# Kernel tuning notes

Measured on AMD Instinct MI355X. Metric: run time of the kernel, lower is better.

The kernel has to match this reference:

```python
import jax, jax.numpy as jnp
import numpy as np

B, S, F, EMB, HID = 64, 2048, 40, 128, 256


def setup_inputs() -> dict:
    key = jax.random.key(0)
    ks = jax.random.split(key, 12)
    sc_in = 1.0 / np.sqrt(F)
    sc_h = 1.0 / np.sqrt(HID)
    n = lambda k, shape, sc: (jax.random.normal(k, shape, jnp.float32) * sc)
    return {
        "in_states": jax.random.normal(ks[0], (B, S, F), jnp.float32),
        "W_in": n(ks[1], (EMB, F), sc_in),
        "b_in": jnp.zeros((EMB,), jnp.float32),  # bias init to 0 in original
        "W_ih0": n(ks[2], (4 * HID, EMB), sc_h),
        "W_hh0": n(ks[3], (4 * HID, HID), sc_h),
        "b_ih0": n(ks[4], (4 * HID,), sc_h),
        "b_hh0": n(ks[5], (4 * HID,), sc_h),
        "W_ih1": n(ks[6], (4 * HID, HID), sc_h),
        "W_hh1": n(ks[7], (4 * HID, HID), sc_h),
        "b_ih1": n(ks[8], (4 * HID,), sc_h),
        "b_hh1": n(ks[9], (4 * HID,), sc_h),
        "W_out": n(ks[10], (1, HID), sc_h),
        "b_out": jnp.zeros((1,), jnp.float32),  # bias init to 0 in original
    }


def _lstm_layer(x, W_ih, W_hh, b_ih, b_hh):
    # x: [B, S, D_in]; returns hs: [B, S, H], final (h, c)
    Bb = x.shape[0]
    H = W_hh.shape[1]
    # Precompute input contribution for all timesteps (one big GEMM).
    gx = jnp.einsum('bsd,gd->bsg', x, W_ih) + b_ih + b_hh  # [B, S, 4H]

    def step(carry, gxt):
        h, c = carry
        g = gxt + h @ W_hh.T  # [B, 4H]
        i, f, gg, o = jnp.split(g, 4, axis=-1)  # PyTorch gate order i,f,g,o
        i = jax.nn.sigmoid(i)
        f = jax.nn.sigmoid(f)
        gg = jnp.tanh(gg)
        o = jax.nn.sigmoid(o)
        c = f * c + i * gg
        h = o * jnp.tanh(c)
        return (h, c), h

    init = (jnp.zeros((Bb, H), x.dtype), jnp.zeros((Bb, H), x.dtype))
    (h, c), hs = jax.lax.scan(step, init, jnp.swapaxes(gx, 0, 1))
    return jnp.swapaxes(hs, 0, 1), (h, c)


def reference(in_states, W_in, b_in, W_ih0, W_hh0, b_ih0, b_hh0,
              W_ih1, W_hh1, b_ih1, b_hh1, W_out, b_out):
    # Input projection applied to every timestep (equivalent to per-step Linear).
    x = jnp.einsum('bsf,ef->bse', in_states, W_in) + b_in  # [B, S, EMB]
    y, _ = _lstm_layer(x, W_ih0, W_hh0, b_ih0, b_hh0)
    y, _ = _lstm_layer(y, W_ih1, W_hh1, b_ih1, b_hh1)
    out = jnp.einsum('bsh,oh->bso', y, W_out) + b_out  # [B, S, 1]
    return out[..., 0]  # [B, S], matches torch.t(outputs)
```

## Files before the change

### kernel.cpp

```cpp
#include <hip/hip_runtime.h>


#define Sz    2048
#define PIPE  4
#define NG    4
#define NJ    8

typedef __attribute__((ext_vector_type(8))) short short8;
typedef __attribute__((ext_vector_type(4))) float f32x4;

#define PUB0_U64 0
#define PUB1_U64 65536
#define CFLG_U32 262144
#define WS_U32   262176

#define HA_HI 0
#define HA_LO 8448
#define HB_HI 16896
#define HB_LO 25344
#define IN_HI 33792
#define IN_LO 36096
#define GBUF  38400
#define SMEM_BYTES 46848
#define WCOMB_OFF 16896

__device__ __forceinline__ unsigned short bf16_rne(float f) {
  unsigned u = __float_as_uint(f);
  u += 0x7FFFu + ((u >> 16) & 1u);
  return (unsigned short)(u >> 16);
}
__device__ __forceinline__ float sigm(float x) { return 1.f / (1.f + __expf(-x)); }
__device__ __forceinline__ float tanh_f(float x) { return 1.f - 2.f / (__expf(2.f * x) + 1.f); }

__device__ __forceinline__ bool load_stage(const unsigned long long* __restrict__ src,
                                           unsigned tagExp, char* hi, char* lo, int tid) {
  unsigned long long v[16];
#pragma unroll
  for (int kt = 0; kt < 8; ++kt) {
    v[kt * 2]     = __hip_atomic_load(src + kt * 512 + tid,       __ATOMIC_RELAXED, __HIP_MEMORY_SCOPE_AGENT);
    v[kt * 2 + 1] = __hip_atomic_load(src + kt * 512 + 256 + tid, __ATOMIC_RELAXED, __HIP_MEMORY_SCOPE_AGENT);
  }
  bool ok = true;
#pragma unroll
  for (int kt = 0; kt < 8; ++kt) {
#pragma unroll
    for (int hh = 0; hh < 2; ++hh) {
      unsigned long long x = v[kt * 2 + hh];
      ok &= ((unsigned)(x >> 32) == tagExp);
      unsigned pk = (unsigned)x;
      int e = tid + hh * 256;
      int m = e >> 5, col = kt * 32 + (e & 31);
      *(short*)(hi + m * 528 + col * 2) = (short)(pk >> 16);
      *(short*)(lo + m * 528 + col * 2) = (short)(pk & 0xffffu);
    }
  }
  return ok;
}

__global__ void zero_kernel(unsigned* __restrict__ ws, float* __restrict__ out) {
  int i = blockIdx.x * 256 + threadIdx.x;
  if (i < WS_U32) ws[i] = 0u;
  if (i < 64 * Sz) out[i] = 0.f;
}

__global__ __launch_bounds__(256, 1) void lstm_persist(
    const float* __restrict__ xin, const float* __restrict__ W_in,
    const float* __restrict__ b_in, const float* __restrict__ W_ih0,
    const float* __restrict__ W_hh0, const float* __restrict__ b_ih0,
    const float* __restrict__ b_hh0, const float* __restrict__ W_ih1,
    const float* __restrict__ W_hh1, const float* __restrict__ b_ih1,
    const float* __restrict__ b_hh1, const float* __restrict__ W_out,
    const float* __restrict__ b_out, float* __restrict__ out,
    unsigned* __restrict__ ws) {
  const int bx = blockIdx.x;
  const int g = bx & 7;
  if (g >= NG) return;
  const int idx = bx >> 3;
  const int layer = idx >> 3;
  const int p = idx & 7;
  const int tid = (int)threadIdx.x;
  const int w = tid >> 6;
  const int lane = tid & 63;
  const int q = lane >> 4;
  const int n16 = lane & 15;

  __shared__ __align__(16) char smem[SMEM_BYTES];

  const int row0 = w * 256 + p * 32 + n16;
  const int row1 = row0 + 16;

  short8 wf_rec[8][2];
  short8 wf_in2[8][2];
  short8 wf_cmb[2][2];
  float bias0 = 0.f, bias1 = 0.f;

  {
    const float* Wrec = layer ? W_hh1 : W_hh0;
#pragma unroll
    for (int kt = 0; kt < 8; ++kt) {
#pragma unroll
      for (int u = 0; u < 2; ++u) {
        const int row = u ? row1 : row0;
        const float* src = Wrec + (size_t)row * 256 + kt * 32 + q * 8;
        union { short8 v; unsigned short s[8]; } fr;
#pragma unroll
        for (int j = 0; j < 8; ++j) fr.s[j] = bf16_rne(src[j]);
        wf_rec[kt][u] = fr.v;
      }
    }
  }
  if (layer == 1) {
#pragma unroll
    for (int kt = 0; kt < 8; ++kt) {
#pragma unroll
      for (int u = 0; u < 2; ++u) {
        const int row = u ? row1 : row0;
        const float* src = W_ih1 + (size_t)row * 256 + kt * 32 + q * 8;
        union { short8 v; unsigned short s[8]; } fr;
#pragma unroll
        for (int j = 0; j < 8; ++j) fr.s[j] = bf16_rne(src[j]);
        wf_in2[kt][u] = fr.v;
      }
    }
    bias0 = b_ih1[row0] + b_hh1[row0];
    bias1 = b_ih1[row1] + b_hh1[row1];
  } else {
    float* wcomb = (float*)(smem + WCOMB_OFF);
    for (int i = tid; i < 128 * 40; i += 256) {
      int rl = i / 40, f = i - rl * 40;
      int gate = rl >> 5, rr = rl & 31;
      int arow = gate * 256 + p * 32 + rr;
      const float* wi = W_ih0 + (size_t)arow * 128;
      float s = 0.f;
      for (int e = 0; e < 128; ++e) s += wi[e] * W_in[e * 40 + f];
      wcomb[rl * 40 + f] = s;
    }
    __syncthreads();
#pragma unroll
    for (int kt = 0; kt < 2; ++kt) {
#pragma unroll
      for (int u = 0; u < 2; ++u) {
        int rl = w * 32 + u * 16 + n16;
        union { short8 v; unsigned short s[8]; } fr;
#pragma unroll
        for (int j = 0; j < 8; ++j) {
          int k = kt * 32 + q * 8 + j;
          fr.s[j] = (k < 40) ? bf16_rne(wcomb[rl * 40 + k]) : (unsigned short)0;
        }
        wf_cmb[kt][u] = fr.v;
      }
    }
    {
      const float* wi0 = W_ih0 + (size_t)row0 * 128;
      const float* wi1 = W_ih0 + (size_t)row1 * 128;
      float s0 = 0.f, s1 = 0.f;
      for (int e = 0; e < 128; ++e) { s0 += wi0[e] * b_in[e]; s1 += wi1[e] * b_in[e]; }
      bias0 = s0 + b_ih0[row0] + b_hh0[row0];
      bias1 = s1 + b_ih0[row1] + b_hh0[row1];
    }
    __syncthreads();
    for (int i = tid; i < 2304; i += 256) *((short*)(smem + IN_HI) + i) = 0;
    __syncthreads();
  }

  float c0 = 0.f, c1 = 0.f;
  float wo = 0.f, bo = 0.f;
  if (layer == 1) { wo = W_out[p * 32 + (tid & 31)]; bo = b_out[0]; }

  unsigned long long* const pub0 = (unsigned long long*)ws + PUB0_U64;
  unsigned long long* const pub1 = (unsigned long long*)ws + PUB1_U64;
  unsigned long long* const pubMy = layer ? pub1 : pub0;
  unsigned* const cflg = ws + CFLG_U32 + g * 8;
  float* gb = (float*)(smem + GBUF);

#pragma unroll 1
  for (int t = 0; t < Sz; ++t) {
    if (layer == 0 && tid < 160) {
      int bb = tid / 10, f4 = tid - bb * 10;
      float4 inv = *(const float4*)(xin + ((size_t)(g * 16 + bb) * Sz + t) * 40 + f4 * 4);
#pragma unroll
      for (int cc = 0; cc < 4; ++cc) {
        float f = ((const float*)&inv)[cc];
        unsigned short hb = bf16_rne(f);
        float fh = __uint_as_float((unsigned)hb << 16);
        unsigned short lb = bf16_rne(f - fh);
        int col = f4 * 4 + cc;
        *(short*)(smem + IN_HI + bb * 144 + col * 2) = (short)hb;
        *(short*)(smem + IN_LO + bb * 144 + col * 2) = (short)lb;
      }
    }

    const int slot_r = (t + PIPE - 1) % PIPE;
    const unsigned long long* srcA = pubMy + (size_t)((g * PIPE + slot_r) * NJ) * 512;
    const unsigned long long* srcB = pub0 + (size_t)((g * PIPE + (t % PIPE)) * NJ) * 512;
    const unsigned tagA = (unsigned)t;
    const unsigned tagB = (unsigned)(t + 1);
    for (;;) {
      bool ok = load_stage(srcA, tagA, smem + HA_HI, smem + HA_LO, tid);
      if (layer == 1) {
        ok &= load_stage(srcB, tagB, smem + HB_HI, smem + HB_LO, tid);
      } else if (tid < 8) {
        unsigned c = __hip_atomic_load(cflg + tid, __ATOMIC_RELAXED, __HIP_MEMORY_SCOPE_AGENT);
        ok &= ((int)c >= t - 3);
      }
      if (__syncthreads_and(ok)) break;
    }
    if (layer == 1 && tid == 0)
      __hip_atomic_store(cflg + p, (unsigned)(t + 1), __ATOMIC_RELAXED, __HIP_MEMORY_SCOPE_AGENT);

    f32x4 acc0 = {0.f, 0.f, 0.f, 0.f};
    f32x4 acc1 = {0.f, 0.f, 0.f, 0.f};
    const int arow = n16 * 528;
    const int kcol = q * 8;
#pragma unroll
    for (int kt = 0; kt < 8; ++kt) {
      short8 aH = *(const short8*)(smem + HA_HI + arow + (kt * 32 + kcol) * 2);
      short8 aL = *(const short8*)(smem + HA_LO + arow + (kt * 32 + kcol) * 2);
      acc0 = __builtin_amdgcn_mfma_f32_16x16x32_bf16(aH, wf_rec[kt][0], acc0, 0, 0, 0);
      acc0 = __builtin_amdgcn_mfma_f32_16x16x32_bf16(aL, wf_rec[kt][0], acc0, 0, 0, 0);
      acc1 = __builtin_amdgcn_mfma_f32_16x16x32_bf16(aH, wf_rec[kt][1], acc1, 0, 0, 0);
      acc1 = __builtin_amdgcn_mfma_f32_16x16x32_bf16(aL, wf_rec[kt][1], acc1, 0, 0, 0);
    }
    if (layer == 1) {
#pragma unroll
      for (int kt = 0; kt < 8; ++kt) {
        short8 aH = *(const short8*)(smem + HB_HI + arow + (kt * 32 + kcol) * 2);
        short8 aL = *(const short8*)(smem + HB_LO + arow + (kt * 32 + kcol) * 2);
        acc0 = __builtin_amdgcn_mfma_f32_16x16x32_bf16(aH, wf_in2[kt][0], acc0, 0, 0, 0);
        acc0 = __builtin_amdgcn_mfma_f32_16x16x32_bf16(aL, wf_in2[kt][0], acc0, 0, 0, 0);
        acc1 = __builtin_amdgcn_mfma_f32_16x16x32_bf16(aH, wf_in2[kt][1], acc1, 0, 0, 0);
        acc1 = __builtin_amdgcn_mfma_f32_16x16x32_bf16(aL, wf_in2[kt][1], acc1, 0, 0, 0);
      }
    } else {
      const int arow_in = n16 * 144;
#pragma unroll
      for (int kt = 0; kt < 2; ++kt) {
        short8 aH = *(const short8*)(smem + IN_HI + arow_in + (kt * 32 + kcol) * 2);
        short8 aL = *(const short8*)(smem + IN_LO + arow_in + (kt * 32 + kcol) * 2);
        acc0 = __builtin_amdgcn_mfma_f32_16x16x32_bf16(aH, wf_cmb[kt][0], acc0, 0, 0, 0);
        acc0 = __builtin_amdgcn_mfma_f32_16x16x32_bf16(aL, wf_cmb[kt][0], acc0, 0, 0, 0);
        acc1 = __builtin_amdgcn_mfma_f32_16x16x32_bf16(aH, wf_cmb[kt][1], acc1, 0, 0, 0);
        acc1 = __builtin_amdgcn_mfma_f32_16x16x32_bf16(aL, wf_cmb[kt][1], acc1, 0, 0, 0);
      }
    }

#pragma unroll
    for (int u = 0; u < 2; ++u) {
      f32x4 a = u ? acc1 : acc0;
      float bs = u ? bias1 : bias0;
#pragma unroll
      for (int r = 0; r < 4; ++r) {
        float v = a[r] + bs;
        v = (w == 2) ? tanh_f(v) : sigm(v);
        gb[w * 528 + (q * 4 + r) * 33 + u * 16 + n16] = v;
      }
    }
    __syncthreads();

    unsigned long long* dst =
        pubMy + (size_t)((g * PIPE + (t % PIPE)) * NJ + p) * 512;
    const unsigned long long tagW = ((unsigned long long)(unsigned)(t + 1)) << 32;
#pragma unroll
    for (int k = 0; k < 2; ++k) {
      int e = tid + k * 256;
      int m = e >> 5, nn = e & 31;
      float iv = gb[0 * 528 + m * 33 + nn];
      float fv = gb[1 * 528 + m * 33 + nn];
      float gv = gb[2 * 528 + m * 33 + nn];
      float ov = gb[3 * 528 + m * 33 + nn];
      float c = k ? c1 : c0;
      c = fv * c + iv * gv;
      float h = ov * tanh_f(c);
      if (k) c1 = c; else c0 = c;
      unsigned short hb = bf16_rne(h);
      float fh = __uint_as_float((unsigned)hb << 16);
      unsigned short lb = bf16_rne(h - fh);
      unsigned pk = ((unsigned)hb << 16) | (unsigned)lb;
      __hip_atomic_store(dst + e, tagW | pk, __ATOMIC_RELAXED, __HIP_MEMORY_SCOPE_AGENT);
      if (layer == 1) {
        float val = h * wo;
#pragma unroll
        for (int off = 16; off; off >>= 1) val += __shfl_down(val, off, 32);
        if (nn == 0) {
          if (p == 0) val += bo;
          atomicAdd(out + (size_t)(g * 16 + m) * Sz + t, val);
        }
      }
    }
  }
}

extern "C" void kernel_launch(void* const* d_in, const int* in_sizes, int n_in,
                              void* d_out, int out_size, void* d_ws, size_t ws_size,
                              hipStream_t stream) {
  const float* xin   = (const float*)d_in[0];
  const float* W_in  = (const float*)d_in[1];
  const float* b_in  = (const float*)d_in[2];
  const float* W_ih0 = (const float*)d_in[3];
  const float* W_hh0 = (const float*)d_in[4];
  const float* b_ih0 = (const float*)d_in[5];
  const float* b_hh0 = (const float*)d_in[6];
  const float* W_ih1 = (const float*)d_in[7];
  const float* W_hh1 = (const float*)d_in[8];
  const float* b_ih1 = (const float*)d_in[9];
  const float* b_hh1 = (const float*)d_in[10];
  const float* W_out = (const float*)d_in[11];
  const float* b_out = (const float*)d_in[12];
  float* out = (float*)d_out;
  unsigned* ws = (unsigned*)d_ws;

  zero_kernel<<<(WS_U32 + 255) / 256, 256, 0, stream>>>(ws, out);
  lstm_persist<<<128, 256, 0, stream>>>(xin, W_in, b_in, W_ih0, W_hh0, b_ih0, b_hh0,
                                        W_ih1, W_hh1, b_ih1, b_hh1, W_out, b_out,
                                        out, ws);
}
```

Measured before the change: 7.873 ms.

## Keep own hidden slice in LDS, poll lightweight flags, prefetch next input

Each block now writes its own hidden-state slice straight into LDS and skips reloading that slice from the global publish buffer. When a polling round fails, blocks spin on a cheap check of one sample word per tile before redoing the full stage load. The input row for the next timestep is also prefetched into registers one step ahead. Together these aim to cut global atomic traffic and latency on the per-step cross-block synchronisation path. The sampled check is not a full completeness test, so the outer full reload still has to validate every tag.

```diff
diff --git a/kernel.cpp b/kernel.cpp
--- a/kernel.cpp
+++ b/kernel.cpp
@@ -33,16 +33,19 @@
 __device__ __forceinline__ float tanh_f(float x) { return 1.f - 2.f / (__expf(2.f * x) + 1.f); }
 
 __device__ __forceinline__ bool load_stage(const unsigned long long* __restrict__ src,
-                                           unsigned tagExp, char* hi, char* lo, int tid) {
+                                           unsigned tagExp, char* hi, char* lo, int tid,
+                                           int skip) {
   unsigned long long v[16];
 #pragma unroll
   for (int kt = 0; kt < 8; ++kt) {
+    if (kt == skip) continue;
     v[kt * 2]     = __hip_atomic_load(src + kt * 512 + tid,       __ATOMIC_RELAXED, __HIP_MEMORY_SCOPE_AGENT);
     v[kt * 2 + 1] = __hip_atomic_load(src + kt * 512 + 256 + tid, __ATOMIC_RELAXED, __HIP_MEMORY_SCOPE_AGENT);
   }
   bool ok = true;
 #pragma unroll
   for (int kt = 0; kt < 8; ++kt) {
+    if (kt == skip) continue;
 #pragma unroll
     for (int hh = 0; hh < 2; ++hh) {
       unsigned long long x = v[kt * 2 + hh];
@@ -160,7 +163,14 @@
     }
     __syncthreads();
     for (int i = tid; i < 2304; i += 256) *((short*)(smem + IN_HI) + i) = 0;
-    __syncthreads();
+  }
+
+#pragma unroll
+  for (int k = 0; k < 2; ++k) {
+    int e = tid + k * 256;
+    int m = e >> 5, col = p * 32 + (e & 31);
+    *(short*)(smem + HA_HI + m * 528 + col * 2) = 0;
+    *(short*)(smem + HA_LO + m * 528 + col * 2) = 0;
   }
 
   float c0 = 0.f, c1 = 0.f;
@@ -173,14 +183,19 @@
   unsigned* const cflg = ws + CFLG_U32 + g * 8;
   float* gb = (float*)(smem + GBUF);
 
+  float4 inreg = {0.f, 0.f, 0.f, 0.f};
+  int bb = 0, f4 = 0;
+  if (layer == 0 && tid < 160) {
+    bb = tid / 10; f4 = tid - bb * 10;
+    inreg = *(const float4*)(xin + ((size_t)(g * 16 + bb) * Sz + 0) * 40 + f4 * 4);
+  }
+
 #pragma unroll 1
   for (int t = 0; t < Sz; ++t) {
     if (layer == 0 && tid < 160) {
-      int bb = tid / 10, f4 = tid - bb * 10;
-      float4 inv = *(const float4*)(xin + ((size_t)(g * 16 + bb) * Sz + t) * 40 + f4 * 4);
 #pragma unroll
       for (int cc = 0; cc < 4; ++cc) {
-        float f = ((const float*)&inv)[cc];
+        float f = ((const float*)&inreg)[cc];
         unsigned short hb = bf16_rne(f);
         float fh = __uint_as_float((unsigned)hb << 16);
         unsigned short lb = bf16_rne(f - fh);
@@ -188,6 +203,8 @@
         *(short*)(smem + IN_HI + bb * 144 + col * 2) = (short)hb;
         *(short*)(smem + IN_LO + bb * 144 + col * 2) = (short)lb;
       }
+      int tn = (t + 1 < Sz) ? t + 1 : t;
+      inreg = *(const float4*)(xin + ((size_t)(g * 16 + bb) * Sz + tn) * 40 + f4 * 4);
     }
 
     const int slot_r = (t + PIPE - 1) % PIPE;
@@ -195,15 +212,34 @@
     const unsigned long long* srcB = pub0 + (size_t)((g * PIPE + (t % PIPE)) * NJ) * 512;
     const unsigned tagA = (unsigned)t;
     const unsigned tagB = (unsigned)(t + 1);
+    const int ktS = tid >> 5;
+    const int wS = 256 + (tid & 31) * 8;
     for (;;) {
-      bool ok = load_stage(srcA, tagA, smem + HA_HI, smem + HA_LO, tid);
+      bool ok = load_stage(srcA, tagA, smem + HA_HI, smem + HA_LO, tid, p);
       if (layer == 1) {
-        ok &= load_stage(srcB, tagB, smem + HB_HI, smem + HB_LO, tid);
+        ok &= load_stage(srcB, tagB, smem + HB_HI, smem + HB_LO, tid, -1);
       } else if (tid < 8) {
         unsigned c = __hip_atomic_load(cflg + tid, __ATOMIC_RELAXED, __HIP_MEMORY_SCOPE_AGENT);
         ok &= ((int)c >= t - 3);
       }
       if (__syncthreads_and(ok)) break;
+      for (;;) {
+        bool okc = true;
+        if (ktS != p) {
+          unsigned long long xa = __hip_atomic_load(srcA + ktS * 512 + wS,
+                                                    __ATOMIC_RELAXED, __HIP_MEMORY_SCOPE_AGENT);
+          okc = ((unsigned)(xa >> 32) == tagA);
+        }
+        if (layer == 1) {
+          unsigned long long xb = __hip_atomic_load(srcB + ktS * 512 + wS,
+                                                    __ATOMIC_RELAXED, __HIP_MEMORY_SCOPE_AGENT);
+          okc &= ((unsigned)(xb >> 32) == tagB);
+        } else if (tid < 8) {
+          unsigned c = __hip_atomic_load(cflg + tid, __ATOMIC_RELAXED, __HIP_MEMORY_SCOPE_AGENT);
+          okc &= ((int)c >= t - 3);
+        }
+        if (__syncthreads_and(okc)) break;
+      }
     }
     if (layer == 1 && tid == 0)
       __hip_atomic_store(cflg + p, (unsigned)(t + 1), __ATOMIC_RELAXED, __HIP_MEMORY_SCOPE_AGENT);
@@ -277,6 +313,8 @@
       unsigned short lb = bf16_rne(h - fh);
       unsigned pk = ((unsigned)hb << 16) | (unsigned)lb;
       __hip_atomic_store(dst + e, tagW | pk, __ATOMIC_RELAXED, __HIP_MEMORY_SCOPE_AGENT);
+      *(short*)(smem + HA_HI + m * 528 + (p * 32 + nn) * 2) = (short)hb;
+      *(short*)(smem + HA_LO + m * 528 + (p * 32 + nn) * 2) = (short)lb;
       if (layer == 1) {
         float val = h * wo;
 #pragma unroll
```

Result: slower. 10.98 ms (+39.5%).

## Poll only pending hidden-state tiles, self-write own slice, prefetch inputs

Applied to the files above, without the earlier changes.

The spin-wait now tracks which 32-column tiles of the previous hidden state are still pending and re-polls only those, copying each tile into shared memory once its tag matches. Each block writes its own freshly computed h slice straight into shared memory instead of reading it back through global atomics. The next timestep's input is prefetched into registers and converted during the first poll iteration, overlapping the global load with synchronization. This trims global traffic and latency on the per-step critical path, at the cost of more registers and extra control flow in the polling loop.

```diff
diff --git a/kernel.cpp b/kernel.cpp
--- a/kernel.cpp
+++ b/kernel.cpp
@@ -32,29 +32,37 @@
 __device__ __forceinline__ float sigm(float x) { return 1.f / (1.f + __expf(-x)); }
 __device__ __forceinline__ float tanh_f(float x) { return 1.f - 2.f / (__expf(2.f * x) + 1.f); }
 
-__device__ __forceinline__ bool load_stage(const unsigned long long* __restrict__ src,
-                                           unsigned tagExp, char* hi, char* lo, int tid) {
-  unsigned long long v[16];
-#pragma unroll
-  for (int kt = 0; kt < 8; ++kt) {
-    v[kt * 2]     = __hip_atomic_load(src + kt * 512 + tid,       __ATOMIC_RELAXED, __HIP_MEMORY_SCOPE_AGENT);
-    v[kt * 2 + 1] = __hip_atomic_load(src + kt * 512 + 256 + tid, __ATOMIC_RELAXED, __HIP_MEMORY_SCOPE_AGENT);
-  }
-  bool ok = true;
-#pragma unroll
-  for (int kt = 0; kt < 8; ++kt) {
-#pragma unroll
-    for (int hh = 0; hh < 2; ++hh) {
-      unsigned long long x = v[kt * 2 + hh];
-      ok &= ((unsigned)(x >> 32) == tagExp);
-      unsigned pk = (unsigned)x;
-      int e = tid + hh * 256;
-      int m = e >> 5, col = kt * 32 + (e & 31);
-      *(short*)(hi + m * 528 + col * 2) = (short)(pk >> 16);
-      *(short*)(lo + m * 528 + col * 2) = (short)(pk & 0xffffu);
-    }
-  }
-  return ok;
+__device__ __forceinline__ void poll_issue(const unsigned long long* __restrict__ src,
+                                           int tid, unsigned pend,
+                                           unsigned long long* v0, unsigned long long* v1) {
+#pragma unroll
+  for (int kt = 0; kt < 8; ++kt)
+    if (pend & (1u << kt)) {
+      v0[kt] = __hip_atomic_load(src + kt * 512 + tid,       __ATOMIC_RELAXED, __HIP_MEMORY_SCOPE_AGENT);
+      v1[kt] = __hip_atomic_load(src + kt * 512 + 256 + tid, __ATOMIC_RELAXED, __HIP_MEMORY_SCOPE_AGENT);
+    }
+}
+
+__device__ __forceinline__ unsigned poll_check(unsigned tagExp, char* hi, char* lo,
+                                               int tid, unsigned pend,
+                                               const unsigned long long* v0,
+                                               const unsigned long long* v1) {
+#pragma unroll
+  for (int kt = 0; kt < 8; ++kt)
+    if (pend & (1u << kt)) {
+      unsigned long long x0 = v0[kt], x1 = v1[kt];
+      if (((unsigned)(x0 >> 32) == tagExp) & ((unsigned)(x1 >> 32) == tagExp)) {
+        unsigned pk0 = (unsigned)x0, pk1 = (unsigned)x1;
+        int m0 = tid >> 5, col = kt * 32 + (tid & 31);
+        *(short*)(hi + m0 * 528 + col * 2) = (short)(pk0 >> 16);
+        *(short*)(lo + m0 * 528 + col * 2) = (short)(pk0 & 0xffffu);
+        int m1 = m0 + 8;
+        *(short*)(hi + m1 * 528 + col * 2) = (short)(pk1 >> 16);
+        *(short*)(lo + m1 * 528 + col * 2) = (short)(pk1 & 0xffffu);
+        pend &= ~(1u << kt);
+      }
+    }
+  return pend;
 }
 
 __global__ void zero_kernel(unsigned* __restrict__ ws, float* __restrict__ out) {
@@ -160,7 +168,14 @@
     }
     __syncthreads();
     for (int i = tid; i < 2304; i += 256) *((short*)(smem + IN_HI) + i) = 0;
-    __syncthreads();
+  }
+
+#pragma unroll
+  for (int k = 0; k < 2; ++k) {
+    int e = tid + k * 256;
+    int m = e >> 5, col = p * 32 + (e & 31);
+    *(short*)(smem + HA_HI + m * 528 + col * 2) = 0;
+    *(short*)(smem + HA_LO + m * 528 + col * 2) = 0;
   }
 
   float c0 = 0.f, c1 = 0.f;
@@ -173,35 +188,53 @@
   unsigned* const cflg = ws + CFLG_U32 + g * 8;
   float* gb = (float*)(smem + GBUF);
 
+  float4 inreg = {0.f, 0.f, 0.f, 0.f};
+  int bb = 0, f4 = 0;
+  if (layer == 0 && tid < 160) {
+    bb = tid / 10; f4 = tid - bb * 10;
+    inreg = *(const float4*)(xin + ((size_t)(g * 16 + bb) * Sz + 0) * 40 + f4 * 4);
+  }
+
 #pragma unroll 1
   for (int t = 0; t < Sz; ++t) {
-    if (layer == 0 && tid < 160) {
-      int bb = tid / 10, f4 = tid - bb * 10;
-      float4 inv = *(const float4*)(xin + ((size_t)(g * 16 + bb) * Sz + t) * 40 + f4 * 4);
-#pragma unroll
-      for (int cc = 0; cc < 4; ++cc) {
-        float f = ((const float*)&inv)[cc];
-        unsigned short hb = bf16_rne(f);
-        float fh = __uint_as_float((unsigned)hb << 16);
-        unsigned short lb = bf16_rne(f - fh);
-        int col = f4 * 4 + cc;
-        *(short*)(smem + IN_HI + bb * 144 + col * 2) = (short)hb;
-        *(short*)(smem + IN_LO + bb * 144 + col * 2) = (short)lb;
-      }
-    }
-
     const int slot_r = (t + PIPE - 1) % PIPE;
     const unsigned long long* srcA = pubMy + (size_t)((g * PIPE + slot_r) * NJ) * 512;
     const unsigned long long* srcB = pub0 + (size_t)((g * PIPE + (t % PIPE)) * NJ) * 512;
     const unsigned tagA = (unsigned)t;
     const unsigned tagB = (unsigned)(t + 1);
-    for (;;) {
-      bool ok = load_stage(srcA, tagA, smem + HA_HI, smem + HA_LO, tid);
+
+    unsigned pendA = 0xFFu ^ (1u << p);
+    unsigned pendB = (layer == 1) ? 0xFFu : 0u;
+    for (int it = 0;; ++it) {
+      unsigned long long a0[8], a1[8], b0[8], b1[8];
+      poll_issue(srcA, tid, pendA, a0, a1);
+      if (layer == 1) poll_issue(srcB, tid, pendB, b0, b1);
+      unsigned cfv = 0;
+      if (layer == 0 && tid < 8)
+        cfv = __hip_atomic_load(cflg + tid, __ATOMIC_RELAXED, __HIP_MEMORY_SCOPE_AGENT);
+
+      if (it == 0 && layer == 0 && tid < 160) {
+#pragma unroll
+        for (int cc = 0; cc < 4; ++cc) {
+          float f = ((const float*)&inreg)[cc];
+          unsigned short hb = bf16_rne(f);
+          float fh = __uint_as_float((unsigned)hb << 16);
+          unsigned short lb = bf16_rne(f - fh);
+          int col = f4 * 4 + cc;
+          *(short*)(smem + IN_HI + bb * 144 + col * 2) = (short)hb;
+          *(short*)(smem + IN_LO + bb * 144 + col * 2) = (short)lb;
+        }
+        int tn = (t + 1 < Sz) ? t + 1 : t;
+        inreg = *(const float4*)(xin + ((size_t)(g * 16 + bb) * Sz + tn) * 40 + f4 * 4);
+      }
+
+      pendA = poll_check(tagA, smem + HA_HI, smem + HA_LO, tid, pendA, a0, a1);
+      bool ok = (pendA == 0);
       if (layer == 1) {
-        ok &= load_stage(srcB, tagB, smem + HB_HI, smem + HB_LO, tid);
+        pendB = poll_check(tagB, smem + HB_HI, smem + HB_LO, tid, pendB, b0, b1);
+        ok &= (pendB == 0);
       } else if (tid < 8) {
-        unsigned c = __hip_atomic_load(cflg + tid, __ATOMIC_RELAXED, __HIP_MEMORY_SCOPE_AGENT);
-        ok &= ((int)c >= t - 3);
+        ok &= ((int)cfv >= t - 3);
       }
       if (__syncthreads_and(ok)) break;
     }
@@ -277,6 +310,8 @@
       unsigned short lb = bf16_rne(h - fh);
       unsigned pk = ((unsigned)hb << 16) | (unsigned)lb;
       __hip_atomic_store(dst + e, tagW | pk, __ATOMIC_RELAXED, __HIP_MEMORY_SCOPE_AGENT);
+      *(short*)(smem + HA_HI + m * 528 + (p * 32 + nn) * 2) = (short)hb;
+      *(short*)(smem + HA_LO + m * 528 + (p * 32 + nn) * 2) = (short)lb;
       if (layer == 1) {
         float val = h * wo;
 #pragma unroll
```

Result: slower. 10.05 ms (+27.6%).

## Fuse both LSTM layers into each block with a one-step wavefront skew

Applied to the files above, without the earlier changes.

Each persistent block now computes both layer 0 at step t and layer 1 at step t-1, instead of using separate blocks per layer. This halves the grid to 64 blocks and keeps all three recurrent and input weight sets in registers. Layer 1 reuses the layer-0 h already staged in shared memory, so it no longer needs a separate cross-block load. The cost is serializing two layers' MFMA and gate work per block per step, which adds roughly 48 more short8 registers per thread and an extra barrier.

```diff
diff --git a/kernel.cpp b/kernel.cpp
--- a/kernel.cpp
+++ b/kernel.cpp
@@ -75,9 +75,7 @@
   const int bx = blockIdx.x;
   const int g = bx & 7;
   if (g >= NG) return;
-  const int idx = bx >> 3;
-  const int layer = idx >> 3;
-  const int p = idx & 7;
+  const int p = bx >> 3;
   const int tid = (int)threadIdx.x;
   const int w = tid >> 6;
   const int lane = tid & 63;
@@ -89,42 +87,36 @@
   const int row0 = w * 256 + p * 32 + n16;
   const int row1 = row0 + 16;
 
-  short8 wf_rec[8][2];
+  short8 wf_rec0[8][2];
+  short8 wf_rec1[8][2];
   short8 wf_in2[8][2];
   short8 wf_cmb[2][2];
-  float bias0 = 0.f, bias1 = 0.f;
+  float b0L0, b1L0, b0L1, b1L1;
+
+#pragma unroll
+  for (int kt = 0; kt < 8; ++kt) {
+#pragma unroll
+    for (int u = 0; u < 2; ++u) {
+      const int row = u ? row1 : row0;
+      const float* s0 = W_hh0 + (size_t)row * 256 + kt * 32 + q * 8;
+      const float* s1 = W_hh1 + (size_t)row * 256 + kt * 32 + q * 8;
+      const float* s2 = W_ih1 + (size_t)row * 256 + kt * 32 + q * 8;
+      union { short8 v; unsigned short s[8]; } f0, f1, f2;
+#pragma unroll
+      for (int j = 0; j < 8; ++j) {
+        f0.s[j] = bf16_rne(s0[j]);
+        f1.s[j] = bf16_rne(s1[j]);
+        f2.s[j] = bf16_rne(s2[j]);
+      }
+      wf_rec0[kt][u] = f0.v;
+      wf_rec1[kt][u] = f1.v;
+      wf_in2[kt][u]  = f2.v;
+    }
+  }
+  b0L1 = b_ih1[row0] + b_hh1[row0];
+  b1L1 = b_ih1[row1] + b_hh1[row1];
 
   {
-    const float* Wrec = layer ? W_hh1 : W_hh0;
-#pragma unroll
-    for (int kt = 0; kt < 8; ++kt) {
-#pragma unroll
-      for (int u = 0; u < 2; ++u) {
-        const int row = u ? row1 : row0;
-        const float* src = Wrec + (size_t)row * 256 + kt * 32 + q * 8;
-        union { short8 v; unsigned short s[8]; } fr;
-#pragma unroll
-        for (int j = 0; j < 8; ++j) fr.s[j] = bf16_rne(src[j]);
-        wf_rec[kt][u] = fr.v;
-      }
-    }
-  }
-  if (layer == 1) {
-#pragma unroll
-    for (int kt = 0; kt < 8; ++kt) {
-#pragma unroll
-      for (int u = 0; u < 2; ++u) {
-        const int row = u ? row1 : row0;
-        const float* src = W_ih1 + (size_t)row * 256 + kt * 32 + q * 8;
-        union { short8 v; unsigned short s[8]; } fr;
-#pragma unroll
-        for (int j = 0; j < 8; ++j) fr.s[j] = bf16_rne(src[j]);
-        wf_in2[kt][u] = fr.v;
-      }
-    }
-    bias0 = b_ih1[row0] + b_hh1[row0];
-    bias1 = b_ih1[row1] + b_hh1[row1];
-  } else {
     float* wcomb = (float*)(smem + WCOMB_OFF);
     for (int i = tid; i < 128 * 40; i += 256) {
       int rl = i / 40, f = i - rl * 40;
@@ -155,27 +147,31 @@
       const float* wi1 = W_ih0 + (size_t)row1 * 128;
       float s0 = 0.f, s1 = 0.f;
       for (int e = 0; e < 128; ++e) { s0 += wi0[e] * b_in[e]; s1 += wi1[e] * b_in[e]; }
-      bias0 = s0 + b_ih0[row0] + b_hh0[row0];
-      bias1 = s1 + b_ih0[row1] + b_hh0[row1];
+      b0L0 = s0 + b_ih0[row0] + b_hh0[row0];
+      b1L0 = s1 + b_ih0[row1] + b_hh0[row1];
     }
     __syncthreads();
     for (int i = tid; i < 2304; i += 256) *((short*)(smem + IN_HI) + i) = 0;
     __syncthreads();
   }
 
-  float c0 = 0.f, c1 = 0.f;
-  float wo = 0.f, bo = 0.f;
-  if (layer == 1) { wo = W_out[p * 32 + (tid & 31)]; bo = b_out[0]; }
+  float cL0_0 = 0.f, cL0_1 = 0.f;
+  float cL1_0 = 0.f, cL1_1 = 0.f;
+  const float wo = W_out[p * 32 + (tid & 31)];
+  const float bo = b_out[0];
 
   unsigned long long* const pub0 = (unsigned long long*)ws + PUB0_U64;
   unsigned long long* const pub1 = (unsigned long long*)ws + PUB1_U64;
-  unsigned long long* const pubMy = layer ? pub1 : pub0;
   unsigned* const cflg = ws + CFLG_U32 + g * 8;
   float* gb = (float*)(smem + GBUF);
 
 #pragma unroll 1
-  for (int t = 0; t < Sz; ++t) {
-    if (layer == 0 && tid < 160) {
+  for (int t = 0; t < Sz + 1; ++t) {
+    const bool doL0 = (t < Sz);
+    const int tL = t - 1;
+    const bool doL1 = (tL >= 0);
+
+    if (doL0 && tid < 160) {
       int bb = tid / 10, f4 = tid - bb * 10;
       float4 inv = *(const float4*)(xin + ((size_t)(g * 16 + bb) * Sz + t) * 40 + f4 * 4);
 #pragma unroll
@@ -190,48 +186,38 @@
       }
     }
 
-    const int slot_r = (t + PIPE - 1) % PIPE;
-    const unsigned long long* srcA = pubMy + (size_t)((g * PIPE + slot_r) * NJ) * 512;
-    const unsigned long long* srcB = pub0 + (size_t)((g * PIPE + (t % PIPE)) * NJ) * 512;
-    const unsigned tagA = (unsigned)t;
-    const unsigned tagB = (unsigned)(t + 1);
+    const unsigned long long* srcA0 =
+        pub0 + (size_t)((g * PIPE + (t + PIPE - 1) % PIPE) * NJ) * 512;
+    const unsigned long long* srcA1 =
+        pub1 + (size_t)((g * PIPE + (tL - 1 + PIPE * 2) % PIPE) * NJ) * 512;
     for (;;) {
-      bool ok = load_stage(srcA, tagA, smem + HA_HI, smem + HA_LO, tid);
-      if (layer == 1) {
-        ok &= load_stage(srcB, tagB, smem + HB_HI, smem + HB_LO, tid);
-      } else if (tid < 8) {
+      bool ok = load_stage(srcA0, (unsigned)t, smem + HA_HI, smem + HA_LO, tid);
+      if (doL1)
+        ok &= load_stage(srcA1, (unsigned)tL, smem + HB_HI, smem + HB_LO, tid);
+      if (tid < 8) {
         unsigned c = __hip_atomic_load(cflg + tid, __ATOMIC_RELAXED, __HIP_MEMORY_SCOPE_AGENT);
-        ok &= ((int)c >= t - 3);
+        ok &= ((int)c >= t - 2);
       }
       if (__syncthreads_and(ok)) break;
     }
-    if (layer == 1 && tid == 0)
+    if (tid == 0)
       __hip_atomic_store(cflg + p, (unsigned)(t + 1), __ATOMIC_RELAXED, __HIP_MEMORY_SCOPE_AGENT);
 
-    f32x4 acc0 = {0.f, 0.f, 0.f, 0.f};
-    f32x4 acc1 = {0.f, 0.f, 0.f, 0.f};
     const int arow = n16 * 528;
     const int kcol = q * 8;
-#pragma unroll
-    for (int kt = 0; kt < 8; ++kt) {
-      short8 aH = *(const short8*)(smem + HA_HI + arow + (kt * 32 + kcol) * 2);
-      short8 aL = *(const short8*)(smem + HA_LO + arow + (kt * 32 + kcol) * 2);
-      acc0 = __builtin_amdgcn_mfma_f32_16x16x32_bf16(aH, wf_rec[kt][0], acc0, 0, 0, 0);
-      acc0 = __builtin_amdgcn_mfma_f32_16x16x32_bf16(aL, wf_rec[kt][0], acc0, 0, 0, 0);
-      acc1 = __builtin_amdgcn_mfma_f32_16x16x32_bf16(aH, wf_rec[kt][1], acc1, 0, 0, 0);
-      acc1 = __builtin_amdgcn_mfma_f32_16x16x32_bf16(aL, wf_rec[kt][1], acc1, 0, 0, 0);
-    }
-    if (layer == 1) {
+
+    if (doL0) {
+      f32x4 acc0 = {0.f, 0.f, 0.f, 0.f};
+      f32x4 acc1 = {0.f, 0.f, 0.f, 0.f};
 #pragma unroll
       for (int kt = 0; kt < 8; ++kt) {
-        short8 aH = *(const short8*)(smem + HB_HI + arow + (kt * 32 + kcol) * 2);
-        short8 aL = *(const short8*)(smem + HB_LO + arow + (kt * 32 + kcol) * 2);
-        acc0 = __builtin_amdgcn_mfma_f32_16x16x32_bf16(aH, wf_in2[kt][0], acc0, 0, 0, 0);
-        acc0 = __builtin_amdgcn_mfma_f32_16x16x32_bf16(aL, wf_in2[kt][0], acc0, 0, 0, 0);
-        acc1 = __builtin_amdgcn_mfma_f32_16x16x32_bf16(aH, wf_in2[kt][1], acc1, 0, 0, 0);
-        acc1 = __builtin_amdgcn_mfma_f32_16x16x32_bf16(aL, wf_in2[kt][1], acc1, 0, 0, 0);
-      }
-    } else {
+        short8 aH = *(const short8*)(smem + HA_HI + arow + (kt * 32 + kcol) * 2);
+        short8 aL = *(const short8*)(smem + HA_LO + arow + (kt * 32 + kcol) * 2);
+        acc0 = __builtin_amdgcn_mfma_f32_16x16x32_bf16(aH, wf_rec0[kt][0], acc0, 0, 0, 0);
+        acc0 = __builtin_amdgcn_mfma_f32_16x16x32_bf16(aL, wf_rec0[kt][0], acc0, 0, 0, 0);
+        acc1 = __builtin_amdgcn_mfma_f32_16x16x32_bf16(aH, wf_rec0[kt][1], acc1, 0, 0, 0);
+        acc1 = __builtin_amdgcn_mfma_f32_16x16x32_bf16(aL, wf_rec0[kt][1], acc1, 0, 0, 0);
+      }
       const int arow_in = n16 * 144;
 #pragma unroll
       for (int kt = 0; kt < 2; ++kt) {
@@ -242,48 +228,101 @@
         acc1 = __builtin_amdgcn_mfma_f32_16x16x32_bf16(aH, wf_cmb[kt][1], acc1, 0, 0, 0);
         acc1 = __builtin_amdgcn_mfma_f32_16x16x32_bf16(aL, wf_cmb[kt][1], acc1, 0, 0, 0);
       }
-    }
-
-#pragma unroll
-    for (int u = 0; u < 2; ++u) {
-      f32x4 a = u ? acc1 : acc0;
-      float bs = u ? bias1 : bias0;
-#pragma unroll
-      for (int r = 0; r < 4; ++r) {
-        float v = a[r] + bs;
-        v = (w == 2) ? tanh_f(v) : sigm(v);
-        gb[w * 528 + (q * 4 + r) * 33 + u * 16 + n16] = v;
-      }
-    }
-    __syncthreads();
-
-    unsigned long long* dst =
-        pubMy + (size_t)((g * PIPE + (t % PIPE)) * NJ + p) * 512;
-    const unsigned long long tagW = ((unsigned long long)(unsigned)(t + 1)) << 32;
-#pragma unroll
-    for (int k = 0; k < 2; ++k) {
-      int e = tid + k * 256;
-      int m = e >> 5, nn = e & 31;
-      float iv = gb[0 * 528 + m * 33 + nn];
-      float fv = gb[1 * 528 + m * 33 + nn];
-      float gv = gb[2 * 528 + m * 33 + nn];
-      float ov = gb[3 * 528 + m * 33 + nn];
-      float c = k ? c1 : c0;
-      c = fv * c + iv * gv;
-      float h = ov * tanh_f(c);
-      if (k) c1 = c; else c0 = c;
-      unsigned short hb = bf16_rne(h);
-      float fh = __uint_as_float((unsigned)hb << 16);
-      unsigned short lb = bf16_rne(h - fh);
-      unsigned pk = ((unsigned)hb << 16) | (unsigned)lb;
-      __hip_atomic_store(dst + e, tagW | pk, __ATOMIC_RELAXED, __HIP_MEMORY_SCOPE_AGENT);
-      if (layer == 1) {
+#pragma unroll
+      for (int u = 0; u < 2; ++u) {
+        f32x4 a = u ? acc1 : acc0;
+        float bs = u ? b1L0 : b0L0;
+#pragma unroll
+        for (int r = 0; r < 4; ++r) {
+          float v = a[r] + bs;
+          v = (w == 2) ? tanh_f(v) : sigm(v);
+          gb[w * 528 + (q * 4 + r) * 33 + u * 16 + n16] = v;
+        }
+      }
+      __syncthreads();
+      unsigned long long* dst =
+          pub0 + (size_t)((g * PIPE + (t % PIPE)) * NJ + p) * 512;
+      const unsigned long long tagW = ((unsigned long long)(unsigned)(t + 1)) << 32;
+#pragma unroll
+      for (int k = 0; k < 2; ++k) {
+        int e = tid + k * 256;
+        int m = e >> 5, nn = e & 31;
+        float iv = gb[0 * 528 + m * 33 + nn];
+        float fv = gb[1 * 528 + m * 33 + nn];
+        float gv = gb[2 * 528 + m * 33 + nn];
+        float ov = gb[3 * 528 + m * 33 + nn];
+        float c = k ? cL0_1 : cL0_0;
+        c = fv * c + iv * gv;
+        float h = ov * tanh_f(c);
+        if (k) cL0_1 = c; else cL0_0 = c;
+        unsigned short hb = bf16_rne(h);
+        float fh = __uint_as_float((unsigned)hb << 16);
+        unsigned short lb = bf16_rne(h - fh);
+        unsigned pk = ((unsigned)hb << 16) | (unsigned)lb;
+        __hip_atomic_store(dst + e, tagW | pk, __ATOMIC_RELAXED, __HIP_MEMORY_SCOPE_AGENT);
+      }
+    }
+
+    if (doL1) {
+      f32x4 acc0 = {0.f, 0.f, 0.f, 0.f};
+      f32x4 acc1 = {0.f, 0.f, 0.f, 0.f};
+#pragma unroll
+      for (int kt = 0; kt < 8; ++kt) {
+        short8 aH = *(const short8*)(smem + HB_HI + arow + (kt * 32 + kcol) * 2);
+        short8 aL = *(const short8*)(smem + HB_LO + arow + (kt * 32 + kcol) * 2);
+        acc0 = __builtin_amdgcn_mfma_f32_16x16x32_bf16(aH, wf_rec1[kt][0], acc0, 0, 0, 0);
+        acc0 = __builtin_amdgcn_mfma_f32_16x16x32_bf16(aL, wf_rec1[kt][0], acc0, 0, 0, 0);
+        acc1 = __builtin_amdgcn_mfma_f32_16x16x32_bf16(aH, wf_rec1[kt][1], acc1, 0, 0, 0);
+        acc1 = __builtin_amdgcn_mfma_f32_16x16x32_bf16(aL, wf_rec1[kt][1], acc1, 0, 0, 0);
+      }
+#pragma unroll
+      for (int kt = 0; kt < 8; ++kt) {
+        short8 aH = *(const short8*)(smem + HA_HI + arow + (kt * 32 + kcol) * 2);
+        short8 aL = *(const short8*)(smem + HA_LO + arow + (kt * 32 + kcol) * 2);
+        acc0 = __builtin_amdgcn_mfma_f32_16x16x32_bf16(aH, wf_in2[kt][0], acc0, 0, 0, 0);
+        acc0 = __builtin_amdgcn_mfma_f32_16x16x32_bf16(aL, wf_in2[kt][0], acc0, 0, 0, 0);
+        acc1 = __builtin_amdgcn_mfma_f32_16x16x32_bf16(aH, wf_in2[kt][1], acc1, 0, 0, 0);
+        acc1 = __builtin_amdgcn_mfma_f32_16x16x32_bf16(aL, wf_in2[kt][1], acc1, 0, 0, 0);
+      }
+      __syncthreads();
+#pragma unroll
+      for (int u = 0; u < 2; ++u) {
+        f32x4 a = u ? acc1 : acc0;
+        float bs = u ? b1L1 : b0L1;
+#pragma unroll
+        for (int r = 0; r < 4; ++r) {
+          float v = a[r] + bs;
+          v = (w == 2) ? tanh_f(v) : sigm(v);
+          gb[w * 528 + (q * 4 + r) * 33 + u * 16 + n16] = v;
+        }
+      }
+      __syncthreads();
+      unsigned long long* dst =
+          pub1 + (size_t)((g * PIPE + (tL % PIPE)) * NJ + p) * 512;
+      const unsigned long long tagW = ((unsigned long long)(unsigned)(tL + 1)) << 32;
+#pragma unroll
+      for (int k = 0; k < 2; ++k) {
+        int e = tid + k * 256;
+        int m = e >> 5, nn = e & 31;
+        float iv = gb[0 * 528 + m * 33 + nn];
+        float fv = gb[1 * 528 + m * 33 + nn];
+        float gv = gb[2 * 528 + m * 33 + nn];
+        float ov = gb[3 * 528 + m * 33 + nn];
+        float c = k ? cL1_1 : cL1_0;
+        c = fv * c + iv * gv;
+        float h = ov * tanh_f(c);
+        if (k) cL1_1 = c; else cL1_0 = c;
+        unsigned short hb = bf16_rne(h);
+        float fh = __uint_as_float((unsigned)hb << 16);
+        unsigned short lb = bf16_rne(h - fh);
+        unsigned pk = ((unsigned)hb << 16) | (unsigned)lb;
+        __hip_atomic_store(dst + e, tagW | pk, __ATOMIC_RELAXED, __HIP_MEMORY_SCOPE_AGENT);
         float val = h * wo;
 #pragma unroll
         for (int off = 16; off; off >>= 1) val += __shfl_down(val, off, 32);
         if (nn == 0) {
           if (p == 0) val += bo;
-          atomicAdd(out + (size_t)(g * 16 + m) * Sz + t, val);
+          atomicAdd(out + (size_t)(g * 16 + m) * Sz + tL, val);
         }
       }
     }
@@ -310,7 +349,7 @@
   unsigned* ws = (unsigned*)d_ws;
 
   zero_kernel<<<(WS_U32 + 255) / 256, 256, 0, stream>>>(ws, out);
-  lstm_persist<<<128, 256, 0, stream>>>(xin, W_in, b_in, W_ih0, W_hh0, b_ih0, b_hh0,
-                                        W_ih1, W_hh1, b_ih1, b_hh1, W_out, b_out,
-                                        out, ws);
-}
+  lstm_persist<<<64, 256, 0, stream>>>(xin, W_in, b_in, W_ih0, W_hh0, b_ih0, b_hh0,
+                                       W_ih1, W_hh1, b_ih1, b_hh1, W_out, b_out,
+                                       out, ws);
+}
```

After: 11.63 ms. 47.7% more time.
